# Kernel optimization log

Hardware: AMD Instinct MI355X
Metric: run time of the kernel (lower is better)

The kernel has to match this reference:

```python
import jax, jax.numpy as jnp
import numpy as np

# --- dims / constants ---
T, N, SD, TD, A, H = 64, 512, 64, 64, 32, 2048
REPEAT = 2
IN_DIM = SD + TD
DT, TAU_MEM, TAU_SYN = 1e-3, 5e-3, 2e-3
DCY_M = float(np.exp(-DT / TAU_MEM))   # membrane decay exp(-dt/tau_mem)
DCY_S = float(np.exp(-DT / TAU_SYN))   # synaptic decay exp(-dt/tau_syn)
SCL_M = 1.0 - DCY_M
BETA = 100.0  # SigmoidSpike surrogate steepness

@jax.custom_vjp
def spike(x):
    # forward: hard threshold (binary spike)
    return (x > 0).astype(x.dtype)

def _spike_fwd(x):
    return spike(x), x

def _spike_bwd(x, g):
    s = jax.nn.sigmoid(BETA * x)
    return (g * BETA * s * (1.0 - s),)

spike.defvjp(_spike_fwd, _spike_bwd)

def setup_inputs() -> dict:
    key = jax.random.key(0)
    ks = jax.random.split(key, 8)
    f32 = jnp.float32
    state = jax.random.normal(ks[0], (T, N, SD), dtype=f32)
    target = jax.random.normal(ks[1], (T, N, TD), dtype=f32)
    # fluctuation-driven centered-normal init ~ N(0, 1/fan_in)
    Wi = jax.random.normal(ks[2], (IN_DIM, H), dtype=f32) / np.sqrt(IN_DIM)
    bi = jnp.zeros((H,), dtype=f32)
    Vr = jax.random.normal(ks[3], (H, H), dtype=f32) / np.sqrt(H)
    Wf = jax.random.normal(ks[4], (H, H), dtype=f32) / np.sqrt(H)
    bf = jnp.zeros((H,), dtype=f32)
    Wo = jax.random.normal(ks[5], (H, 2 * A), dtype=f32) / np.sqrt(H)
    bo = jnp.zeros((2 * A,), dtype=f32)
    return {"state": state, "target": target, "Wi": Wi, "bi": bi,
            "Vr": Vr, "Wf": Wf, "bf": bf, "Wo": Wo, "bo": bo}

def _run(state, target, Wi, bi, Vr, Wf, bf, Wo, bo):
    x_seq = jnp.concatenate([state, target], axis=-1)        # (T, N, IN_DIM)
    x_seq = jnp.repeat(x_seq, REPEAT, axis=0)                 # (T*REPEAT, N, IN_DIM)

    def step(carry, xt):
        syn1, mem1, s1, syn2, mem2, s2, synr, memr = carry
        # recurrent LIF layer: feedforward + recurrent input
        I1 = xt @ Wi + bi + s1 @ Vr
        nmem1 = (DCY_M * mem1 + SCL_M * syn1) * (1.0 - s1)    # reset by last spikes
        nsyn1 = DCY_S * syn1 + I1
        ns1 = spike(nmem1 - 1.0)                              # threshold = 1
        # feedforward LIF layer
        I2 = ns1 @ Wf + bf
        nmem2 = (DCY_M * mem2 + SCL_M * syn2) * (1.0 - s2)
        nsyn2 = DCY_S * syn2 + I2
        ns2 = spike(nmem2 - 1.0)
        # non-spiking readout pool (leaky integrator)
        Ir = ns2 @ Wo + bo
        nmemr = DCY_M * memr + SCL_M * synr
        nsynr = DCY_S * synr + Ir
        new_carry = (nsyn1, nmem1, ns1, nsyn2, nmem2, ns2, nsynr, nmemr)
        return new_carry, nmemr

    z = lambda d: jnp.zeros((N, d), dtype=state.dtype)
    carry0 = (z(H), z(H), z(H), z(H), z(H), z(H), z(2 * A), z(2 * A))
    _, ro = jax.lax.scan(step, carry0, x_seq)                 # (T*REPEAT, N, 2A)
    # TimeAverageReadoutGroup: mean over the repeat_input micro-steps
    ro = ro.reshape(T, REPEAT, N, 2 * A).mean(axis=1)         # (T, N, 2A)
    mu, logvar = jnp.split(ro, 2, axis=-1)
    return mu, logvar

def reference(state, target, Wi, bi, Vr, Wf, bf, Wo, bo):
    return _run(state, target, Wi, bi, Vr, Wf, bf, Wo, bo)
```

## Files before the change

### kernel.cpp

```cpp
#include <hip/hip_runtime.h>
#include <stdint.h>


typedef unsigned long long u64;
typedef unsigned int u32;
typedef float f32x4 __attribute__((ext_vector_type(4)));

#define NB 512
#define HD 2048
#define NSTEPS 128
#define THREADS 512
#define NBLK 256
#define COLS 256
#define SPB 16
#define NWPS 32
#define LSTN 832

#define DMc 0.8187307530779818f
#define DSc 0.6065306597126334f
#define SMc 0.18126924692201818f

#define OFF_M1W 0
#define SZ_M1W ((size_t)2 * NB * NWPS * 8)
#define OFF_M2H (OFF_M1W + SZ_M1W)
#define SZ_M2H ((size_t)NSTEPS * NB * NWPS * 8)
#define OFF_FLAG (OFF_M2H + SZ_M2H)
#define SZ_FLAG (32 * 32 * 4)
#define OFF_CNT (OFF_FLAG + SZ_FLAG)
#define OFF_DONE (OFF_CNT + 64)
#define OFF_PK (((size_t)(OFF_DONE + 4) + 4194303) & ~(size_t)4194303)
#define SZ_PK ((size_t)8 * HD * 512 * 4)
#define OFF_XW (((OFF_PK + SZ_PK) + 255) & ~(size_t)255)
#define SZ_XW ((size_t)64 * NB * HD * 4)

#define HWREG_XCC_ID (20 | ((4 - 1) << 11))

__global__ void init_ws(u64* __restrict__ m1W, u32* __restrict__ flags,
                        u32* __restrict__ cnt, u32* __restrict__ done) {
  int i = blockIdx.x * 256 + threadIdx.x;
  if (i < 2 * NB * NWPS) m1W[i] = 0ULL;
  if (i < 32 * 32) flags[i] = 0u;
  if (i < 8) cnt[i] = 0u;
  if (i == 0) *done = 0u;
}

__global__ __launch_bounds__(256) void pack_kernel(
    const float* __restrict__ Vr, const float* __restrict__ Wf,
    float* __restrict__ PK) {
  const int k = blockIdx.x;
  const int tid = threadIdx.x;
  for (int c = tid; c < HD; c += 256) {
    int xcd = c >> 8, cc = c & 255;
    size_t base = ((size_t)xcd * HD + k) * 512;
    __builtin_nontemporal_store(Vr[(size_t)k * HD + c], &PK[base + cc]);
    __builtin_nontemporal_store(Wf[(size_t)k * HD + c], &PK[base + 256 + cc]);
  }
}

__global__ __launch_bounds__(256) void xw_kernel(
    const float* __restrict__ state, const float* __restrict__ target,
    const float* __restrict__ Wi, const float* __restrict__ bi,
    float* __restrict__ XW) {
  __shared__ float xl[16][128];
  const int tid = threadIdx.x;
  const int col = blockIdx.x * 256 + tid;
  const int r0 = blockIdx.y * 16;

  for (int idx = tid; idx < 16 * 128; idx += 256) {
    int r = idx >> 7, k = idx & 127;
    int gg = r0 + r;
    int t = gg >> 9, n = gg & 511;
    float v = (k < 64) ? state[((size_t)(t * NB + n)) * 64 + k]
                       : target[((size_t)(t * NB + n)) * 64 + (k - 64)];
    xl[r][k] = v;
  }
  __syncthreads();

  float acc[16];
  float b = bi[col];
#pragma unroll
  for (int r = 0; r < 16; ++r) acc[r] = b;
  for (int k = 0; k < 128; ++k) {
    float w = Wi[(size_t)k * HD + col];
#pragma unroll
    for (int r = 0; r < 16; ++r) acc[r] = fmaf(xl[r][k], w, acc[r]);
  }
#pragma unroll
  for (int r = 0; r < 16; ++r)
    __builtin_nontemporal_store(acc[r], &XW[(size_t)(r0 + r) * HD + col]);
}

__device__ __forceinline__ u64 spread4(u64 x) {
  x &= 0xffffULL;
  x = (x | (x << 24)) & 0x000000FF000000FFULL;
  x = (x | (x << 12)) & 0x000F000F000F000FULL;
  x = (x | (x << 6))  & 0x0303030303030303ULL;
  x = (x | (x << 3))  & 0x1111111111111111ULL;
  return x;
}

__device__ __forceinline__ u64 pack_word(u64 B0, u64 B1, u64 B2, u64 B3, int q) {
  int sh = q * 16;
  return spread4(B0 >> sh) | (spread4(B1 >> sh) << 1) |
         (spread4(B2 >> sh) << 2) | (spread4(B3 >> sh) << 3);
}

__device__ __forceinline__ void build_ab(const u64* __restrict__ mA,
                                         const u64* __restrict__ mB,
                                         uint16_t* __restrict__ lstA,
                                         uint16_t* __restrict__ lstB,
                                         int lane, int& totA, int& totB) {
  const int hf = lane >> 5, wl = lane & 31;
  const u64* src = hf ? mB : mA;
  u64 w = __hip_atomic_load(src + wl, __ATOMIC_RELAXED,
                            __HIP_MEMORY_SCOPE_AGENT);
  int pc = __popcll(w);
  int pre = pc;
#pragma unroll
  for (int off = 1; off < 32; off <<= 1) {
    int v = __shfl_up(pre, off, 32);
    if (wl >= off) pre += v;
  }
  int excl = pre - pc;
  totA = __shfl(pre, 31);
  totB = __shfl(pre, 63);
  uint16_t* lw = hf ? lstB : lstA;
  int kb = wl << 6;
  while (w) {
    int b = __builtin_ctzll(w);
    w &= w - 1;
    if (excl < LSTN) lw[excl] = (uint16_t)(kb + b);
    ++excl;
  }
  asm volatile("s_waitcnt lgkmcnt(0)" ::: "memory");
  totA = totA < LSTN ? totA : LSTN;
  totB = totB < LSTN ? totB : LSTN;
}

__device__ __forceinline__ int build_list_ro(const u64* __restrict__ mwords,
                                             uint16_t* __restrict__ lstw,
                                             int lane) {
  u64 w = (lane < NWPS) ? mwords[lane] : 0ULL;
  int pc = __popcll(w);
  int pre = pc;
#pragma unroll
  for (int off = 1; off < 64; off <<= 1) {
    int v = __shfl_up(pre, off);
    if (lane >= off) pre += v;
  }
  int excl = pre - pc;
  int total = __shfl(pre, 63);
  int kb = lane << 6;
  while (w) {
    int b = __builtin_ctzll(w);
    w &= w - 1;
    if (excl < LSTN) lstw[excl] = (uint16_t)(kb + b);
    ++excl;
  }
  asm volatile("s_waitcnt lgkmcnt(0)" ::: "memory");
  return total < LSTN ? total : LSTN;
}

__device__ __forceinline__ u32 lif_update(const float acc[4], float syn[4],
                                          float mem[4], u32 snib) {
  u32 nib = 0;
#pragma unroll
  for (int j = 0; j < 4; ++j) {
    float so = (float)((snib >> j) & 1u);
    float nmem = (DMc * mem[j] + SMc * syn[j]) * (1.0f - so);
    float nsyn = DSc * syn[j] + acc[j];
    mem[j] = nmem;
    syn[j] = nsyn;
    if ((nmem - 1.0f) > 0.0f) nib |= (1u << j);
  }
  return nib;
}

__device__ __forceinline__ void gather_ab(const float* __restrict__ PKb,
                                          const uint16_t* __restrict__ lstA,
                                          int totA,
                                          const uint16_t* __restrict__ lstB,
                                          int totB, float aVA[4], float aWA[4],
                                          float aVB[4], float aWB[4]) {
  int tot = totA > totB ? totA : totB;
  for (int j0 = 0; j0 < tot; j0 += 8) {
    f32x4 va[8], wa[8], vb[8], wb[8];
#pragma unroll
    for (int u = 0; u < 8; ++u) {
      int ia = j0 + u;
      if (ia >= totA) ia = 0;
      size_t offA = ((size_t)lstA[ia]) << 9;
      va[u] = *(const f32x4*)(PKb + offA);
      wa[u] = *(const f32x4*)(PKb + offA + 256);
    }
#pragma unroll
    for (int u = 0; u < 8; ++u) {
      int ib = j0 + u;
      if (ib >= totB) ib = 0;
      size_t offB = ((size_t)lstB[ib]) << 9;
      vb[u] = *(const f32x4*)(PKb + offB);
      wb[u] = *(const f32x4*)(PKb + offB + 256);
    }
#pragma unroll
    for (int u = 0; u < 8; ++u)
      if (j0 + u < totA) {
        aVA[0] += va[u].x; aVA[1] += va[u].y; aVA[2] += va[u].z; aVA[3] += va[u].w;
        aWA[0] += wa[u].x; aWA[1] += wa[u].y; aWA[2] += wa[u].z; aWA[3] += wa[u].w;
      }
#pragma unroll
    for (int u = 0; u < 8; ++u)
      if (j0 + u < totB) {
        aVB[0] += vb[u].x; aVB[1] += vb[u].y; aVB[2] += vb[u].z; aVB[3] += vb[u].w;
        aWB[0] += wb[u].x; aWB[1] += wb[u].y; aWB[2] += wb[u].z; aWB[3] += wb[u].w;
      }
  }
}

template <int UXW>
__global__ __launch_bounds__(THREADS, 2) void rsnn_coop(
    const float* __restrict__ state, const float* __restrict__ target,
    const float* __restrict__ Wi, const float* __restrict__ bi,
    const float* __restrict__ Vr, const float* __restrict__ Wf,
    const float* __restrict__ bf, const float* __restrict__ Wo,
    const float* __restrict__ bo, float* __restrict__ out,
    char* __restrict__ wsb) {
  __shared__ float Wi_s[128 * COLS];
  __shared__ uint16_t lstA_s[8][LSTN];
  __shared__ uint16_t lstB_s[8][LSTN];
  __shared__ int sh_xcd, sh_rank;

  u64* m1W = (u64*)(wsb + OFF_M1W);
  u64* m2H = (u64*)(wsb + OFF_M2H);
  u32* flags = (u32*)(wsb + OFF_FLAG);
  u32* cnt = (u32*)(wsb + OFF_CNT);
  u32* done = (u32*)(wsb + OFF_DONE);
  const float* PK = (const float*)(wsb + OFF_PK);
  const float* XW = (const float*)(wsb + OFF_XW);

  const int tid = threadIdx.x;
  const int wv = tid >> 6;
  const int lane = tid & 63;

  if (tid == 0) {
    int x = __builtin_amdgcn_s_getreg(HWREG_XCC_ID) & 7;
    sh_xcd = x;
    sh_rank = atomicAdd(&cnt[x], 1u) & 31;
  }
  __syncthreads();
  const int xcd = sh_xcd;
  const int g = sh_rank;
  const int c0 = xcd * COLS;
  const int sA = g * SPB + wv * 2, sB = sA + 1;

  if constexpr (!UXW) {
    for (int i = tid; i < 128 * COLS; i += THREADS) {
      int k = i >> 8, c = i & 255;
      Wi_s[i] = Wi[(size_t)k * HD + c0 + c];
    }
  }
  uint16_t* lstA = &lstA_s[wv][0];
  uint16_t* lstB = &lstB_s[wv][0];
  if (lane == 0) { lstA[0] = 0; lstB[0] = 0; }

  float bir[4], bfr[4];
#pragma unroll
  for (int j = 0; j < 4; ++j) {
    bir[j] = bi[c0 + lane * 4 + j];
    bfr[j] = bf[c0 + lane * 4 + j];
  }

  float syn1A[4], mem1A[4], syn2A[4], mem2A[4];
  float syn1B[4], mem1B[4], syn2B[4], mem2B[4];
#pragma unroll
  for (int j = 0; j < 4; ++j) {
    syn1A[j] = 0.f; mem1A[j] = 0.f; syn2A[j] = 0.f; mem2A[j] = 0.f;
    syn1B[j] = 0.f; mem1B[j] = 0.f; syn2B[j] = 0.f; mem2B[j] = 0.f;
  }
  u32 nib1A = 0u, nib1B = 0u, nib2A = 0u, nib2B = 0u;
  float xwA[4], xwB[4];
  f32x4 xwNA, xwNB;

  const float* PKb = PK + (size_t)xcd * HD * 512 + lane * 4;
  const float* XWc = XW + c0 + lane * 4;
  u32* myflag = &flags[g * 32];

  __syncthreads();

  auto compute_xw = [&](int t2) {
#pragma unroll
    for (int j = 0; j < 4; ++j) { xwA[j] = bir[j]; xwB[j] = bir[j]; }
#pragma unroll
    for (int half = 0; half < 2; ++half) {
      const float* pA = (half ? target : state) + ((size_t)t2 * NB + sA) * 64;
      const float* pB = (half ? target : state) + ((size_t)t2 * NB + sB) * 64;
      for (int q = 0; q < 16; ++q) {
        f32x4 xa = *(const f32x4*)(pA + 4 * q);
        f32x4 xb = *(const f32x4*)(pB + 4 * q);
        float xav[4] = {xa.x, xa.y, xa.z, xa.w};
        float xbv[4] = {xb.x, xb.y, xb.z, xb.w};
#pragma unroll
        for (int kj = 0; kj < 4; ++kj) {
          const f32x4 w4 =
              *(const f32x4*)&Wi_s[(half * 64 + 4 * q + kj) * COLS + lane * 4];
          xwA[0] = fmaf(xav[kj], w4.x, xwA[0]);
          xwA[1] = fmaf(xav[kj], w4.y, xwA[1]);
          xwA[2] = fmaf(xav[kj], w4.z, xwA[2]);
          xwA[3] = fmaf(xav[kj], w4.w, xwA[3]);
          xwB[0] = fmaf(xbv[kj], w4.x, xwB[0]);
          xwB[1] = fmaf(xbv[kj], w4.y, xwB[1]);
          xwB[2] = fmaf(xbv[kj], w4.z, xwB[2]);
          xwB[3] = fmaf(xbv[kj], w4.w, xwB[3]);
        }
      }
    }
  };

  if constexpr (UXW) {
    f32x4 a = __builtin_nontemporal_load((const f32x4*)(XWc + (size_t)sA * HD));
    f32x4 b = __builtin_nontemporal_load((const f32x4*)(XWc + (size_t)sB * HD));
    xwA[0] = a.x; xwA[1] = a.y; xwA[2] = a.z; xwA[3] = a.w;
    xwB[0] = b.x; xwB[1] = b.y; xwB[2] = b.z; xwB[3] = b.w;
  } else {
    compute_xw(0);
  }
  nib1A = lif_update(xwA, syn1A, mem1A, 0u);
  nib1B = lif_update(xwB, syn1B, mem1B, 0u);
  {
    u64 E0 = __ballot(nib1A & 1u), E1 = __ballot(nib1A & 2u);
    u64 E2 = __ballot(nib1A & 4u), E3 = __ballot(nib1A & 8u);
    u64 F0 = __ballot(nib1B & 1u), F1 = __ballot(nib1B & 2u);
    u64 F2 = __ballot(nib1B & 4u), F3 = __ballot(nib1B & 8u);
    if (lane < 4)
      __hip_atomic_store(&m1W[(size_t)sA * NWPS + 4 * xcd + lane],
                         pack_word(E0, E1, E2, E3, lane), __ATOMIC_RELAXED,
                         __HIP_MEMORY_SCOPE_AGENT);
    else if (lane < 8)
      __hip_atomic_store(&m1W[(size_t)sB * NWPS + 4 * xcd + (lane - 4)],
                         pack_word(F0, F1, F2, F3, lane - 4), __ATOMIC_RELAXED,
                         __HIP_MEMORY_SCOPE_AGENT);
  }
  if constexpr (UXW) {
    xwNA = __builtin_nontemporal_load(
        (const f32x4*)(XWc + ((size_t)1 * NB + sA) * HD));
    xwNB = __builtin_nontemporal_load(
        (const f32x4*)(XWc + ((size_t)1 * NB + sB) * HD));
  }
  __syncthreads();
  if (tid == 0) {
    __hip_atomic_fetch_add(myflag, 1u, __ATOMIC_RELAXED, __HIP_MEMORY_SCOPE_AGENT);
    while (__hip_atomic_load(myflag, __ATOMIC_RELAXED,
                             __HIP_MEMORY_SCOPE_AGENT) < 8u)
      __builtin_amdgcn_s_sleep(2);
  }
  __syncthreads();

  for (int s = 0; s < NSTEPS; ++s) {
    if (s & 1) {
      if constexpr (UXW) {
        xwA[0] = xwNA.x; xwA[1] = xwNA.y; xwA[2] = xwNA.z; xwA[3] = xwNA.w;
        xwB[0] = xwNB.x; xwB[1] = xwNB.y; xwB[2] = xwNB.z; xwB[3] = xwNB.w;
      } else {
        if (s + 1 < NSTEPS) compute_xw((s + 1) >> 1);
      }
    } else {
      if constexpr (UXW) {
        int t2 = (s >> 1) + 1;
        if (t2 < 64) {
          xwNA = __builtin_nontemporal_load(
              (const f32x4*)(XWc + ((size_t)t2 * NB + sA) * HD));
          xwNB = __builtin_nontemporal_load(
              (const f32x4*)(XWc + ((size_t)t2 * NB + sB) * HD));
        }
      }
    }

    const u64* m1cur = m1W + (size_t)(s & 1) * NB * NWPS;
    u64* m1n = m1W + (size_t)((s + 1) & 1) * NB * NWPS;
    const bool last = (s == NSTEPS - 1);

    int totA, totB;
    build_ab(m1cur + (size_t)sA * NWPS, m1cur + (size_t)sB * NWPS, lstA, lstB,
             lane, totA, totB);

    float aVA[4] = {xwA[0], xwA[1], xwA[2], xwA[3]};
    float aWA[4] = {bfr[0], bfr[1], bfr[2], bfr[3]};
    float aVB[4] = {xwB[0], xwB[1], xwB[2], xwB[3]};
    float aWB[4] = {bfr[0], bfr[1], bfr[2], bfr[3]};
    gather_ab(PKb, lstA, totA, lstB, totB, aVA, aWA, aVB, aWB);

    nib2A = lif_update(aWA, syn2A, mem2A, nib2A);
    nib2B = lif_update(aWB, syn2B, mem2B, nib2B);
    if (!last) {
      nib1A = lif_update(aVA, syn1A, mem1A, nib1A);
      nib1B = lif_update(aVB, syn1B, mem1B, nib1B);
    }
    {
      u64 D0 = __ballot(nib2A & 1u), D1 = __ballot(nib2A & 2u);
      u64 D2 = __ballot(nib2A & 4u), D3 = __ballot(nib2A & 8u);
      u64 G0 = __ballot(nib2B & 1u), G1 = __ballot(nib2B & 2u);
      u64 G2 = __ballot(nib2B & 4u), G3 = __ballot(nib2B & 8u);
      if (lane < 4)
        __hip_atomic_store(&m2H[((size_t)s * NB + sA) * NWPS + 4 * xcd + lane],
                           pack_word(D0, D1, D2, D3, lane), __ATOMIC_RELAXED,
                           __HIP_MEMORY_SCOPE_AGENT);
      else if (lane < 8)
        __hip_atomic_store(
            &m2H[((size_t)s * NB + sB) * NWPS + 4 * xcd + (lane - 4)],
            pack_word(G0, G1, G2, G3, lane - 4), __ATOMIC_RELAXED,
            __HIP_MEMORY_SCOPE_AGENT);
      if (!last) {
        u64 E0 = __ballot(nib1A & 1u), E1 = __ballot(nib1A & 2u);
        u64 E2 = __ballot(nib1A & 4u), E3 = __ballot(nib1A & 8u);
        u64 F0 = __ballot(nib1B & 1u), F1 = __ballot(nib1B & 2u);
        u64 F2 = __ballot(nib1B & 4u), F3 = __ballot(nib1B & 8u);
        if (lane < 4)
          __hip_atomic_store(&m1n[(size_t)sA * NWPS + 4 * xcd + lane],
                             pack_word(E0, E1, E2, E3, lane), __ATOMIC_RELAXED,
                             __HIP_MEMORY_SCOPE_AGENT);
        else if (lane < 8)
          __hip_atomic_store(&m1n[(size_t)sB * NWPS + 4 * xcd + (lane - 4)],
                             pack_word(F0, F1, F2, F3, lane - 4),
                             __ATOMIC_RELAXED, __HIP_MEMORY_SCOPE_AGENT);
      }
    }

    if (!last) {
      __syncthreads();
      if (tid == 0) {
        __hip_atomic_fetch_add(myflag, 1u, __ATOMIC_RELAXED,
                               __HIP_MEMORY_SCOPE_AGENT);
        u32 tgt = 8u * (u32)(s + 2);
        while (__hip_atomic_load(myflag, __ATOMIC_RELAXED,
                                 __HIP_MEMORY_SCOPE_AGENT) < tgt)
          __builtin_amdgcn_s_sleep(2);
      }
      __syncthreads();
    }
  }

  __syncthreads();
  if (tid == 0) {
    __threadfence();
    __hip_atomic_fetch_add(done, 1u, __ATOMIC_RELEASE, __HIP_MEMORY_SCOPE_AGENT);
    while (__hip_atomic_load(done, __ATOMIC_RELAXED,
                             __HIP_MEMORY_SCOPE_AGENT) < (u32)NBLK)
      __builtin_amdgcn_s_sleep(8);
    __threadfence();
  }
  __syncthreads();

  if (wv < 2) {
    const int rsmp = blockIdx.x * 2 + wv;
    const float bor = bo[lane];
    float synr = 0.f, memr = 0.f, roprev = 0.f;
    for (int s = 0; s < NSTEPS; ++s) {
      int total = build_list_ro(m2H + ((size_t)s * NB + rsmp) * NWPS, lstA, lane);
      float a = bor;
      for (int j0 = 0; j0 < total; j0 += 8) {
        float vv[8];
#pragma unroll
        for (int u = 0; u < 8; ++u) {
          int idx = j0 + u;
          if (idx >= total) idx = j0;
          vv[u] = Wo[(((size_t)lstA[idx]) << 6) + lane];
        }
#pragma unroll
        for (int u = 0; u < 8; ++u)
          if (j0 + u < total) a += vv[u];
      }
      float nmemr = DMc * memr + SMc * synr;
      float nsynr = DSc * synr + a;
      memr = nmemr;
      synr = nsynr;
      if (s & 1) {
        float v = 0.5f * (roprev + nmemr);
        size_t base = ((size_t)(s >> 1) * NB + rsmp) * 32;
        if (lane < 32) out[base + lane] = v;
        else out[(size_t)64 * NB * 32 + base + (lane - 32)] = v;
      } else {
        roprev = nmemr;
      }
    }
  }
}

extern "C" void kernel_launch(void* const* d_in, const int* in_sizes, int n_in,
                              void* d_out, int out_size, void* d_ws, size_t ws_size,
                              hipStream_t stream) {
  const float* state  = (const float*)d_in[0];
  const float* target = (const float*)d_in[1];
  const float* Wi     = (const float*)d_in[2];
  const float* bi     = (const float*)d_in[3];
  const float* Vr     = (const float*)d_in[4];
  const float* Wf     = (const float*)d_in[5];
  const float* bf     = (const float*)d_in[6];
  const float* Wo     = (const float*)d_in[7];
  const float* bo     = (const float*)d_in[8];
  float* out = (float*)d_out;
  char* wsb = (char*)d_ws;

  const int use_xw = (ws_size >= OFF_XW + SZ_XW) ? 1 : 0;

  init_ws<<<128, 256, 0, stream>>>((u64*)(wsb + OFF_M1W), (u32*)(wsb + OFF_FLAG),
                                   (u32*)(wsb + OFF_CNT), (u32*)(wsb + OFF_DONE));
  pack_kernel<<<HD, 256, 0, stream>>>(Vr, Wf, (float*)(wsb + OFF_PK));
  if (use_xw)
    xw_kernel<<<dim3(8, 2048), 256, 0, stream>>>(state, target, Wi, bi,
                                                 (float*)(wsb + OFF_XW));

  void* args[] = {(void*)&state, (void*)&target, (void*)&Wi, (void*)&bi,
                  (void*)&Vr, (void*)&Wf, (void*)&bf, (void*)&Wo, (void*)&bo,
                  (void*)&out, (void*)&wsb};
  if (use_xw)
    (void)hipLaunchCooperativeKernel(rsnn_coop<1>, dim3(NBLK), dim3(THREADS),
                                     args, 0, stream);
  else
    (void)hipLaunchCooperativeKernel(rsnn_coop<0>, dim3(NBLK), dim3(THREADS),
                                     args, 0, stream);
}
```

Baseline: 3.578 ms.

## Use one sample per wave, per-XCD step slots, and zero-row padded gather

Each wave now handles one sample instead of two, and blocks grow to 1024 threads with a higher occupancy hint. The shared fetch-add flag barrier becomes per-XCD step slots polled with a min check. The layer-1 spike words are published, and the slot signalled, before the layer-2 update, so peer blocks can start the next step earlier. The gather pads spike lists to a multiple of 8 with an appended zero row, which removes per-element predicates. The list caps are dropped and the shared Wi copy for the non-XW path is removed, trading more register and LDS pressure for less serialization.

```diff
diff --git a/kernel.cpp b/kernel.cpp
--- a/kernel.cpp
+++ b/kernel.cpp
@@ -8,13 +8,15 @@
 
 #define NB 512
 #define HD 2048
+#define ROWS 2049
 #define NSTEPS 128
-#define THREADS 512
+#define THREADS 1024
 #define NBLK 256
 #define COLS 256
 #define SPB 16
 #define NWPS 32
-#define LSTN 832
+#define LSTN 2600
+#define ZROW 2048
 
 #define DMc 0.8187307530779818f
 #define DSc 0.6065306597126334f
@@ -24,22 +26,23 @@
 #define SZ_M1W ((size_t)2 * NB * NWPS * 8)
 #define OFF_M2H (OFF_M1W + SZ_M1W)
 #define SZ_M2H ((size_t)NSTEPS * NB * NWPS * 8)
-#define OFF_FLAG (OFF_M2H + SZ_M2H)
-#define SZ_FLAG (32 * 32 * 4)
-#define OFF_CNT (OFF_FLAG + SZ_FLAG)
+#define OFF_SLOT (OFF_M2H + SZ_M2H)
+#define SZ_SLOT (256 * 128)
+#define OFF_CNT (OFF_SLOT + SZ_SLOT)
 #define OFF_DONE (OFF_CNT + 64)
 #define OFF_PK (((size_t)(OFF_DONE + 4) + 4194303) & ~(size_t)4194303)
-#define SZ_PK ((size_t)8 * HD * 512 * 4)
+#define SZ_PK ((size_t)8 * ROWS * 512 * 4)
 #define OFF_XW (((OFF_PK + SZ_PK) + 255) & ~(size_t)255)
 #define SZ_XW ((size_t)64 * NB * HD * 4)
 
 #define HWREG_XCC_ID (20 | ((4 - 1) << 11))
-
-__global__ void init_ws(u64* __restrict__ m1W, u32* __restrict__ flags,
+#define SLOT(base, g, x) ((base) + ((size_t)((g)*8 + (x)) * 32))
+
+__global__ void init_ws(u64* __restrict__ m1W, u32* __restrict__ slots,
                         u32* __restrict__ cnt, u32* __restrict__ done) {
   int i = blockIdx.x * 256 + threadIdx.x;
   if (i < 2 * NB * NWPS) m1W[i] = 0ULL;
-  if (i < 32 * 32) flags[i] = 0u;
+  if (i < 8192) slots[i] = 0u;
   if (i < 8) cnt[i] = 0u;
   if (i == 0) *done = 0u;
 }
@@ -51,9 +54,11 @@
   const int tid = threadIdx.x;
   for (int c = tid; c < HD; c += 256) {
     int xcd = c >> 8, cc = c & 255;
-    size_t base = ((size_t)xcd * HD + k) * 512;
-    __builtin_nontemporal_store(Vr[(size_t)k * HD + c], &PK[base + cc]);
-    __builtin_nontemporal_store(Wf[(size_t)k * HD + c], &PK[base + 256 + cc]);
+    size_t base = ((size_t)xcd * ROWS + k) * 512;
+    float v = (k < HD) ? Vr[(size_t)k * HD + c] : 0.0f;
+    float w = (k < HD) ? Wf[(size_t)k * HD + c] : 0.0f;
+    __builtin_nontemporal_store(v, &PK[base + cc]);
+    __builtin_nontemporal_store(w, &PK[base + 256 + cc]);
   }
 }
 
@@ -105,36 +110,31 @@
          (spread4(B2 >> sh) << 2) | (spread4(B3 >> sh) << 3);
 }
 
-__device__ __forceinline__ void build_ab(const u64* __restrict__ mA,
-                                         const u64* __restrict__ mB,
-                                         uint16_t* __restrict__ lstA,
-                                         uint16_t* __restrict__ lstB,
-                                         int lane, int& totA, int& totB) {
-  const int hf = lane >> 5, wl = lane & 31;
-  const u64* src = hf ? mB : mA;
-  u64 w = __hip_atomic_load(src + wl, __ATOMIC_RELAXED,
-                            __HIP_MEMORY_SCOPE_AGENT);
+__device__ __forceinline__ int build_one(const u64* __restrict__ mw,
+                                         uint16_t* __restrict__ lst, int lane) {
+  u64 w = 0ULL;
+  if (lane < NWPS)
+    w = __hip_atomic_load((u64*)&mw[lane], __ATOMIC_RELAXED,
+                          __HIP_MEMORY_SCOPE_AGENT);
   int pc = __popcll(w);
   int pre = pc;
 #pragma unroll
-  for (int off = 1; off < 32; off <<= 1) {
-    int v = __shfl_up(pre, off, 32);
-    if (wl >= off) pre += v;
+  for (int off = 1; off < 64; off <<= 1) {
+    int v = __shfl_up(pre, off);
+    if (lane >= off) pre += v;
   }
   int excl = pre - pc;
-  totA = __shfl(pre, 31);
-  totB = __shfl(pre, 63);
-  uint16_t* lw = hf ? lstB : lstA;
-  int kb = wl << 6;
+  int total = __shfl(pre, 63);
+  int kb = lane << 6;
   while (w) {
     int b = __builtin_ctzll(w);
     w &= w - 1;
-    if (excl < LSTN) lw[excl] = (uint16_t)(kb + b);
-    ++excl;
-  }
+    lst[excl++] = (uint16_t)(kb + b);
+  }
+  int r8 = (total + 7) & ~7;
+  if (lane < 8 && total + lane < r8) lst[total + lane] = (uint16_t)ZROW;
   asm volatile("s_waitcnt lgkmcnt(0)" ::: "memory");
-  totA = totA < LSTN ? totA : LSTN;
-  totB = totB < LSTN ? totB : LSTN;
+  return r8;
 }
 
 __device__ __forceinline__ int build_list_ro(const u64* __restrict__ mwords,
@@ -154,11 +154,10 @@
   while (w) {
     int b = __builtin_ctzll(w);
     w &= w - 1;
-    if (excl < LSTN) lstw[excl] = (uint16_t)(kb + b);
-    ++excl;
+    lstw[excl++] = (uint16_t)(kb + b);
   }
   asm volatile("s_waitcnt lgkmcnt(0)" ::: "memory");
-  return total < LSTN ? total : LSTN;
+  return total;
 }
 
 __device__ __forceinline__ u32 lif_update(const float acc[4], float syn[4],
@@ -176,62 +175,39 @@
   return nib;
 }
 
-__device__ __forceinline__ void gather_ab(const float* __restrict__ PKb,
-                                          const uint16_t* __restrict__ lstA,
-                                          int totA,
-                                          const uint16_t* __restrict__ lstB,
-                                          int totB, float aVA[4], float aWA[4],
-                                          float aVB[4], float aWB[4]) {
-  int tot = totA > totB ? totA : totB;
-  for (int j0 = 0; j0 < tot; j0 += 8) {
-    f32x4 va[8], wa[8], vb[8], wb[8];
+__device__ __forceinline__ void gather_one(const float* __restrict__ PKb,
+                                           const uint16_t* __restrict__ lst,
+                                           int r8, float aV[4], float aW[4]) {
+  for (int j0 = 0; j0 < r8; j0 += 8) {
+    f32x4 v[8], w8[8];
 #pragma unroll
     for (int u = 0; u < 8; ++u) {
-      int ia = j0 + u;
-      if (ia >= totA) ia = 0;
-      size_t offA = ((size_t)lstA[ia]) << 9;
-      va[u] = *(const f32x4*)(PKb + offA);
-      wa[u] = *(const f32x4*)(PKb + offA + 256);
+      size_t off = ((size_t)lst[j0 + u]) << 9;
+      v[u] = *(const f32x4*)(PKb + off);
+      w8[u] = *(const f32x4*)(PKb + off + 256);
     }
 #pragma unroll
     for (int u = 0; u < 8; ++u) {
-      int ib = j0 + u;
-      if (ib >= totB) ib = 0;
-      size_t offB = ((size_t)lstB[ib]) << 9;
-      vb[u] = *(const f32x4*)(PKb + offB);
-      wb[u] = *(const f32x4*)(PKb + offB + 256);
-    }
-#pragma unroll
-    for (int u = 0; u < 8; ++u)
-      if (j0 + u < totA) {
-        aVA[0] += va[u].x; aVA[1] += va[u].y; aVA[2] += va[u].z; aVA[3] += va[u].w;
-        aWA[0] += wa[u].x; aWA[1] += wa[u].y; aWA[2] += wa[u].z; aWA[3] += wa[u].w;
-      }
-#pragma unroll
-    for (int u = 0; u < 8; ++u)
-      if (j0 + u < totB) {
-        aVB[0] += vb[u].x; aVB[1] += vb[u].y; aVB[2] += vb[u].z; aVB[3] += vb[u].w;
-        aWB[0] += wb[u].x; aWB[1] += wb[u].y; aWB[2] += wb[u].z; aWB[3] += wb[u].w;
-      }
+      aV[0] += v[u].x; aV[1] += v[u].y; aV[2] += v[u].z; aV[3] += v[u].w;
+      aW[0] += w8[u].x; aW[1] += w8[u].y; aW[2] += w8[u].z; aW[3] += w8[u].w;
+    }
   }
 }
 
 template <int UXW>
-__global__ __launch_bounds__(THREADS, 2) void rsnn_coop(
+__global__ __launch_bounds__(THREADS, 4) void rsnn_coop(
     const float* __restrict__ state, const float* __restrict__ target,
     const float* __restrict__ Wi, const float* __restrict__ bi,
     const float* __restrict__ Vr, const float* __restrict__ Wf,
     const float* __restrict__ bf, const float* __restrict__ Wo,
     const float* __restrict__ bo, float* __restrict__ out,
     char* __restrict__ wsb) {
-  __shared__ float Wi_s[128 * COLS];
-  __shared__ uint16_t lstA_s[8][LSTN];
-  __shared__ uint16_t lstB_s[8][LSTN];
+  __shared__ uint16_t lst_s[16][LSTN];
   __shared__ int sh_xcd, sh_rank;
 
   u64* m1W = (u64*)(wsb + OFF_M1W);
   u64* m2H = (u64*)(wsb + OFF_M2H);
-  u32* flags = (u32*)(wsb + OFF_FLAG);
+  u32* slots = (u32*)(wsb + OFF_SLOT);
   u32* cnt = (u32*)(wsb + OFF_CNT);
   u32* done = (u32*)(wsb + OFF_DONE);
   const float* PK = (const float*)(wsb + OFF_PK);
@@ -250,17 +226,9 @@
   const int xcd = sh_xcd;
   const int g = sh_rank;
   const int c0 = xcd * COLS;
-  const int sA = g * SPB + wv * 2, sB = sA + 1;
-
-  if constexpr (!UXW) {
-    for (int i = tid; i < 128 * COLS; i += THREADS) {
-      int k = i >> 8, c = i & 255;
-      Wi_s[i] = Wi[(size_t)k * HD + c0 + c];
-    }
-  }
-  uint16_t* lstA = &lstA_s[wv][0];
-  uint16_t* lstB = &lstB_s[wv][0];
-  if (lane == 0) { lstA[0] = 0; lstB[0] = 0; }
+  const int smp = g * SPB + wv;
+
+  uint16_t* lst = &lst_s[wv][0];
 
   float bir[4], bfr[4];
 #pragma unroll
@@ -269,170 +237,146 @@
     bfr[j] = bf[c0 + lane * 4 + j];
   }
 
-  float syn1A[4], mem1A[4], syn2A[4], mem2A[4];
-  float syn1B[4], mem1B[4], syn2B[4], mem2B[4];
+  float syn1[4], mem1[4], syn2[4], mem2[4];
 #pragma unroll
   for (int j = 0; j < 4; ++j) {
-    syn1A[j] = 0.f; mem1A[j] = 0.f; syn2A[j] = 0.f; mem2A[j] = 0.f;
-    syn1B[j] = 0.f; mem1B[j] = 0.f; syn2B[j] = 0.f; mem2B[j] = 0.f;
-  }
-  u32 nib1A = 0u, nib1B = 0u, nib2A = 0u, nib2B = 0u;
-  float xwA[4], xwB[4];
-  f32x4 xwNA, xwNB;
-
-  const float* PKb = PK + (size_t)xcd * HD * 512 + lane * 4;
+    syn1[j] = 0.f; mem1[j] = 0.f; syn2[j] = 0.f; mem2[j] = 0.f;
+  }
+  u32 nib1 = 0u, nib2 = 0u;
+  float xw[4];
+  f32x4 xwN;
+
+  const float* PKb = PK + (size_t)xcd * ROWS * 512 + lane * 4;
   const float* XWc = XW + c0 + lane * 4;
-  u32* myflag = &flags[g * 32];
-
-  __syncthreads();
 
   auto compute_xw = [&](int t2) {
 #pragma unroll
-    for (int j = 0; j < 4; ++j) { xwA[j] = bir[j]; xwB[j] = bir[j]; }
+    for (int j = 0; j < 4; ++j) xw[j] = bir[j];
 #pragma unroll
     for (int half = 0; half < 2; ++half) {
-      const float* pA = (half ? target : state) + ((size_t)t2 * NB + sA) * 64;
-      const float* pB = (half ? target : state) + ((size_t)t2 * NB + sB) * 64;
+      const float* p = (half ? target : state) + ((size_t)t2 * NB + smp) * 64;
       for (int q = 0; q < 16; ++q) {
-        f32x4 xa = *(const f32x4*)(pA + 4 * q);
-        f32x4 xb = *(const f32x4*)(pB + 4 * q);
-        float xav[4] = {xa.x, xa.y, xa.z, xa.w};
-        float xbv[4] = {xb.x, xb.y, xb.z, xb.w};
+        f32x4 xq = *(const f32x4*)(p + 4 * q);
+        float xv[4] = {xq.x, xq.y, xq.z, xq.w};
 #pragma unroll
         for (int kj = 0; kj < 4; ++kj) {
-          const f32x4 w4 =
-              *(const f32x4*)&Wi_s[(half * 64 + 4 * q + kj) * COLS + lane * 4];
-          xwA[0] = fmaf(xav[kj], w4.x, xwA[0]);
-          xwA[1] = fmaf(xav[kj], w4.y, xwA[1]);
-          xwA[2] = fmaf(xav[kj], w4.z, xwA[2]);
-          xwA[3] = fmaf(xav[kj], w4.w, xwA[3]);
-          xwB[0] = fmaf(xbv[kj], w4.x, xwB[0]);
-          xwB[1] = fmaf(xbv[kj], w4.y, xwB[1]);
-          xwB[2] = fmaf(xbv[kj], w4.z, xwB[2]);
-          xwB[3] = fmaf(xbv[kj], w4.w, xwB[3]);
+          const f32x4 w4 = *(const f32x4*)&Wi[(size_t)(half * 64 + 4 * q + kj) *
+                                                  HD + c0 + lane * 4];
+          xw[0] = fmaf(xv[kj], w4.x, xw[0]);
+          xw[1] = fmaf(xv[kj], w4.y, xw[1]);
+          xw[2] = fmaf(xv[kj], w4.z, xw[2]);
+          xw[3] = fmaf(xv[kj], w4.w, xw[3]);
         }
       }
     }
   };
 
   if constexpr (UXW) {
-    f32x4 a = __builtin_nontemporal_load((const f32x4*)(XWc + (size_t)sA * HD));
-    f32x4 b = __builtin_nontemporal_load((const f32x4*)(XWc + (size_t)sB * HD));
-    xwA[0] = a.x; xwA[1] = a.y; xwA[2] = a.z; xwA[3] = a.w;
-    xwB[0] = b.x; xwB[1] = b.y; xwB[2] = b.z; xwB[3] = b.w;
+    f32x4 a = __builtin_nontemporal_load(
+        (const f32x4*)(XWc + (size_t)smp * HD));
+    xw[0] = a.x; xw[1] = a.y; xw[2] = a.z; xw[3] = a.w;
   } else {
     compute_xw(0);
   }
-  nib1A = lif_update(xwA, syn1A, mem1A, 0u);
-  nib1B = lif_update(xwB, syn1B, mem1B, 0u);
+  nib1 = lif_update(xw, syn1, mem1, 0u);
   {
-    u64 E0 = __ballot(nib1A & 1u), E1 = __ballot(nib1A & 2u);
-    u64 E2 = __ballot(nib1A & 4u), E3 = __ballot(nib1A & 8u);
-    u64 F0 = __ballot(nib1B & 1u), F1 = __ballot(nib1B & 2u);
-    u64 F2 = __ballot(nib1B & 4u), F3 = __ballot(nib1B & 8u);
+    u64 E0 = __ballot(nib1 & 1u), E1 = __ballot(nib1 & 2u);
+    u64 E2 = __ballot(nib1 & 4u), E3 = __ballot(nib1 & 8u);
     if (lane < 4)
-      __hip_atomic_store(&m1W[(size_t)sA * NWPS + 4 * xcd + lane],
+      __hip_atomic_store(&m1W[(size_t)smp * NWPS + 4 * xcd + lane],
                          pack_word(E0, E1, E2, E3, lane), __ATOMIC_RELAXED,
                          __HIP_MEMORY_SCOPE_AGENT);
-    else if (lane < 8)
-      __hip_atomic_store(&m1W[(size_t)sB * NWPS + 4 * xcd + (lane - 4)],
-                         pack_word(F0, F1, F2, F3, lane - 4), __ATOMIC_RELAXED,
-                         __HIP_MEMORY_SCOPE_AGENT);
-  }
+  }
+  __syncthreads();
+  if (tid == 0)
+    __hip_atomic_store(SLOT(slots, g, xcd), 1u, __ATOMIC_RELAXED,
+                       __HIP_MEMORY_SCOPE_AGENT);
   if constexpr (UXW) {
-    xwNA = __builtin_nontemporal_load(
-        (const f32x4*)(XWc + ((size_t)1 * NB + sA) * HD));
-    xwNB = __builtin_nontemporal_load(
-        (const f32x4*)(XWc + ((size_t)1 * NB + sB) * HD));
+    xwN = __builtin_nontemporal_load(
+        (const f32x4*)(XWc + ((size_t)1 * NB + smp) * HD));
   }
   __syncthreads();
   if (tid == 0) {
-    __hip_atomic_fetch_add(myflag, 1u, __ATOMIC_RELAXED, __HIP_MEMORY_SCOPE_AGENT);
-    while (__hip_atomic_load(myflag, __ATOMIC_RELAXED,
-                             __HIP_MEMORY_SCOPE_AGENT) < 8u)
+    while (true) {
+      u32 mn = 0xffffffffu;
+#pragma unroll
+      for (int x2 = 0; x2 < 8; ++x2) {
+        u32 v = __hip_atomic_load(SLOT(slots, g, x2), __ATOMIC_RELAXED,
+                                  __HIP_MEMORY_SCOPE_AGENT);
+        mn = v < mn ? v : mn;
+      }
+      if (mn >= 1u) break;
       __builtin_amdgcn_s_sleep(2);
+    }
   }
   __syncthreads();
 
   for (int s = 0; s < NSTEPS; ++s) {
+    const bool last = (s == NSTEPS - 1);
     if (s & 1) {
       if constexpr (UXW) {
-        xwA[0] = xwNA.x; xwA[1] = xwNA.y; xwA[2] = xwNA.z; xwA[3] = xwNA.w;
-        xwB[0] = xwNB.x; xwB[1] = xwNB.y; xwB[2] = xwNB.z; xwB[3] = xwNB.w;
+        xw[0] = xwN.x; xw[1] = xwN.y; xw[2] = xwN.z; xw[3] = xwN.w;
       } else {
         if (s + 1 < NSTEPS) compute_xw((s + 1) >> 1);
       }
-    } else {
+    }
+
+    const u64* m1cur = m1W + (size_t)(s & 1) * NB * NWPS;
+    u64* m1n = m1W + (size_t)((s + 1) & 1) * NB * NWPS;
+
+    int r8 = build_one(m1cur + (size_t)smp * NWPS, lst, lane);
+
+    float aV[4] = {xw[0], xw[1], xw[2], xw[3]};
+    float aW[4] = {bfr[0], bfr[1], bfr[2], bfr[3]};
+    gather_one(PKb, lst, r8, aV, aW);
+
+    if (!last) {
+      nib1 = lif_update(aV, syn1, mem1, nib1);
+      u64 E0 = __ballot(nib1 & 1u), E1 = __ballot(nib1 & 2u);
+      u64 E2 = __ballot(nib1 & 4u), E3 = __ballot(nib1 & 8u);
+      if (lane < 4)
+        __hip_atomic_store(&m1n[(size_t)smp * NWPS + 4 * xcd + lane],
+                           pack_word(E0, E1, E2, E3, lane), __ATOMIC_RELAXED,
+                           __HIP_MEMORY_SCOPE_AGENT);
+    }
+    __syncthreads();
+    if (!last && tid == 0)
+      __hip_atomic_store(SLOT(slots, g, xcd), (u32)(s + 2), __ATOMIC_RELAXED,
+                         __HIP_MEMORY_SCOPE_AGENT);
+
+    nib2 = lif_update(aW, syn2, mem2, nib2);
+    {
+      u64 D0 = __ballot(nib2 & 1u), D1 = __ballot(nib2 & 2u);
+      u64 D2 = __ballot(nib2 & 4u), D3 = __ballot(nib2 & 8u);
+      if (lane < 4)
+        __hip_atomic_store(&m2H[((size_t)s * NB + smp) * NWPS + 4 * xcd + lane],
+                           pack_word(D0, D1, D2, D3, lane), __ATOMIC_RELAXED,
+                           __HIP_MEMORY_SCOPE_AGENT);
+    }
+    if ((s & 1) == 0) {
       if constexpr (UXW) {
         int t2 = (s >> 1) + 1;
         if (t2 < 64) {
-          xwNA = __builtin_nontemporal_load(
-              (const f32x4*)(XWc + ((size_t)t2 * NB + sA) * HD));
-          xwNB = __builtin_nontemporal_load(
-              (const f32x4*)(XWc + ((size_t)t2 * NB + sB) * HD));
+          xwN = __builtin_nontemporal_load(
+              (const f32x4*)(XWc + ((size_t)t2 * NB + smp) * HD));
         }
-      }
-    }
-
-    const u64* m1cur = m1W + (size_t)(s & 1) * NB * NWPS;
-    u64* m1n = m1W + (size_t)((s + 1) & 1) * NB * NWPS;
-    const bool last = (s == NSTEPS - 1);
-
-    int totA, totB;
-    build_ab(m1cur + (size_t)sA * NWPS, m1cur + (size_t)sB * NWPS, lstA, lstB,
-             lane, totA, totB);
-
-    float aVA[4] = {xwA[0], xwA[1], xwA[2], xwA[3]};
-    float aWA[4] = {bfr[0], bfr[1], bfr[2], bfr[3]};
-    float aVB[4] = {xwB[0], xwB[1], xwB[2], xwB[3]};
-    float aWB[4] = {bfr[0], bfr[1], bfr[2], bfr[3]};
-    gather_ab(PKb, lstA, totA, lstB, totB, aVA, aWA, aVB, aWB);
-
-    nib2A = lif_update(aWA, syn2A, mem2A, nib2A);
-    nib2B = lif_update(aWB, syn2B, mem2B, nib2B);
-    if (!last) {
-      nib1A = lif_update(aVA, syn1A, mem1A, nib1A);
-      nib1B = lif_update(aVB, syn1B, mem1B, nib1B);
-    }
-    {
-      u64 D0 = __ballot(nib2A & 1u), D1 = __ballot(nib2A & 2u);
-      u64 D2 = __ballot(nib2A & 4u), D3 = __ballot(nib2A & 8u);
-      u64 G0 = __ballot(nib2B & 1u), G1 = __ballot(nib2B & 2u);
-      u64 G2 = __ballot(nib2B & 4u), G3 = __ballot(nib2B & 8u);
-      if (lane < 4)
-        __hip_atomic_store(&m2H[((size_t)s * NB + sA) * NWPS + 4 * xcd + lane],
-                           pack_word(D0, D1, D2, D3, lane), __ATOMIC_RELAXED,
-                           __HIP_MEMORY_SCOPE_AGENT);
-      else if (lane < 8)
-        __hip_atomic_store(
-            &m2H[((size_t)s * NB + sB) * NWPS + 4 * xcd + (lane - 4)],
-            pack_word(G0, G1, G2, G3, lane - 4), __ATOMIC_RELAXED,
-            __HIP_MEMORY_SCOPE_AGENT);
-      if (!last) {
-        u64 E0 = __ballot(nib1A & 1u), E1 = __ballot(nib1A & 2u);
-        u64 E2 = __ballot(nib1A & 4u), E3 = __ballot(nib1A & 8u);
-        u64 F0 = __ballot(nib1B & 1u), F1 = __ballot(nib1B & 2u);
-        u64 F2 = __ballot(nib1B & 4u), F3 = __ballot(nib1B & 8u);
-        if (lane < 4)
-          __hip_atomic_store(&m1n[(size_t)sA * NWPS + 4 * xcd + lane],
-                             pack_word(E0, E1, E2, E3, lane), __ATOMIC_RELAXED,
-                             __HIP_MEMORY_SCOPE_AGENT);
-        else if (lane < 8)
-          __hip_atomic_store(&m1n[(size_t)sB * NWPS + 4 * xcd + (lane - 4)],
-                             pack_word(F0, F1, F2, F3, lane - 4),
-                             __ATOMIC_RELAXED, __HIP_MEMORY_SCOPE_AGENT);
       }
     }
 
     if (!last) {
       __syncthreads();
       if (tid == 0) {
-        __hip_atomic_fetch_add(myflag, 1u, __ATOMIC_RELAXED,
-                               __HIP_MEMORY_SCOPE_AGENT);
-        u32 tgt = 8u * (u32)(s + 2);
-        while (__hip_atomic_load(myflag, __ATOMIC_RELAXED,
-                                 __HIP_MEMORY_SCOPE_AGENT) < tgt)
+        while (true) {
+          u32 mn = 0xffffffffu;
+#pragma unroll
+          for (int x2 = 0; x2 < 8; ++x2) {
+            u32 v = __hip_atomic_load(SLOT(slots, g, x2), __ATOMIC_RELAXED,
+                                      __HIP_MEMORY_SCOPE_AGENT);
+            mn = v < mn ? v : mn;
+          }
+          if (mn >= (u32)(s + 2)) break;
           __builtin_amdgcn_s_sleep(2);
+        }
       }
       __syncthreads();
     }
@@ -454,7 +398,7 @@
     const float bor = bo[lane];
     float synr = 0.f, memr = 0.f, roprev = 0.f;
     for (int s = 0; s < NSTEPS; ++s) {
-      int total = build_list_ro(m2H + ((size_t)s * NB + rsmp) * NWPS, lstA, lane);
+      int total = build_list_ro(m2H + ((size_t)s * NB + rsmp) * NWPS, lst, lane);
       float a = bor;
       for (int j0 = 0; j0 < total; j0 += 8) {
         float vv[8];
@@ -462,7 +406,7 @@
         for (int u = 0; u < 8; ++u) {
           int idx = j0 + u;
           if (idx >= total) idx = j0;
-          vv[u] = Wo[(((size_t)lstA[idx]) << 6) + lane];
+          vv[u] = Wo[(((size_t)lst[idx]) << 6) + lane];
         }
 #pragma unroll
         for (int u = 0; u < 8; ++u)
@@ -501,9 +445,9 @@
 
   const int use_xw = (ws_size >= OFF_XW + SZ_XW) ? 1 : 0;
 
-  init_ws<<<128, 256, 0, stream>>>((u64*)(wsb + OFF_M1W), (u32*)(wsb + OFF_FLAG),
+  init_ws<<<128, 256, 0, stream>>>((u64*)(wsb + OFF_M1W), (u32*)(wsb + OFF_SLOT),
                                    (u32*)(wsb + OFF_CNT), (u32*)(wsb + OFF_DONE));
-  pack_kernel<<<HD, 256, 0, stream>>>(Vr, Wf, (float*)(wsb + OFF_PK));
+  pack_kernel<<<ROWS, 256, 0, stream>>>(Vr, Wf, (float*)(wsb + OFF_PK));
   if (use_xw)
     xw_kernel<<<dim3(8, 2048), 256, 0, stream>>>(state, target, Wi, bi,
                                                  (float*)(wsb + OFF_XW));
```

New measurement: 9.711 ms. 2.71x slower.
